# Kernel optimization log

Measured on AMD Instinct MI355X. Metric: run time of the kernel, lower is better.

The kernel has to match this reference:

```python
import jax, jax.numpy as jnp
import numpy as np

N_NODES = 50000
N_EDGES = 800000
NODE_DIM = 27
HIDDEN = 64
HEADS = 4
CTX = 32
N_BUCKETS = 7
NEG_SLOPE = 0.2


def gat_layer(x, src, dst, W, att_src, att_dst, bias, n_nodes):
    """PyG GATConv with heads=HEADS, concat=False (mean over heads), self-loops already in src/dst."""
    h = (x @ W).reshape(n_nodes, HEADS, HIDDEN)          # [N,H,F]
    a_src = jnp.einsum('nhf,hf->nh', h, att_src)          # [N,H]
    a_dst = jnp.einsum('nhf,hf->nh', h, att_dst)          # [N,H]
    e = a_src[src] + a_dst[dst]                           # [E,H]
    e = jnp.where(e >= 0, e, NEG_SLOPE * e)               # leaky_relu
    # segment softmax over incoming edges of each dst node
    m = jax.ops.segment_max(e, dst, num_segments=n_nodes)
    ex = jnp.exp(e - m[dst])
    denom = jax.ops.segment_sum(ex, dst, num_segments=n_nodes)
    alpha = ex / denom[dst]                               # [E,H]
    msg = h[src] * alpha[:, :, None]                      # [E,H,F]
    out = jax.ops.segment_sum(msg, dst, num_segments=n_nodes)  # [N,H,F]
    return out.mean(axis=1) + bias                        # [N,F]


def _glorot(key, shape, fan_in, fan_out):
    s = jnp.sqrt(6.0 / (fan_in + fan_out)).astype(jnp.float32)
    return jax.random.uniform(key, shape, jnp.float32, -s, s)


def setup_inputs() -> dict:
    key = jax.random.key(0)
    ks = jax.random.split(key, 20)
    x = jax.random.normal(ks[0], (N_NODES, NODE_DIM), jnp.float32)
    edge_index = jax.random.randint(ks[1], (2, N_EDGES), 0, N_NODES)
    donor_emb = jax.random.normal(ks[2], (1, CTX), jnp.float32)
    candidate_indices = jax.random.randint(ks[3], (8192,), 0, N_NODES)
    HF = HEADS * HIDDEN
    return {
        'x': x, 'edge_index': edge_index, 'donor_emb': donor_emb,
        'candidate_indices': candidate_indices,
        'W1': _glorot(ks[4], (NODE_DIM, HF), NODE_DIM, HF),
        'as1': _glorot(ks[5], (HEADS, HIDDEN), HIDDEN, HIDDEN),
        'ad1': _glorot(ks[6], (HEADS, HIDDEN), HIDDEN, HIDDEN),
        'b1': jnp.zeros((HIDDEN,), jnp.float32),
        'W2': _glorot(ks[7], (HIDDEN, HF), HIDDEN, HF),
        'as2': _glorot(ks[8], (HEADS, HIDDEN), HIDDEN, HIDDEN),
        'ad2': _glorot(ks[9], (HEADS, HIDDEN), HIDDEN, HIDDEN),
        'b2': jnp.zeros((HIDDEN,), jnp.float32),
        'sW1': _glorot(ks[10], (HIDDEN + CTX, HIDDEN), HIDDEN + CTX, HIDDEN),
        'sb1': jnp.zeros((HIDDEN,), jnp.float32),
        'sW2': _glorot(ks[11], (HIDDEN, 1), HIDDEN, 1),
        'sb2': jnp.zeros((1,), jnp.float32),
        'lW1': _glorot(ks[12], (HIDDEN + CTX, HIDDEN), HIDDEN + CTX, HIDDEN),
        'lb1': jnp.zeros((HIDDEN,), jnp.float32),
        'lW2': _glorot(ks[13], (HIDDEN, N_BUCKETS), HIDDEN, N_BUCKETS),
        'lb2': jnp.zeros((N_BUCKETS,), jnp.float32),
    }


def reference(x, edge_index, donor_emb, candidate_indices,
              W1, as1, ad1, b1, W2, as2, ad2, b2,
              sW1, sb1, sW2, sb2, lW1, lb1, lW2, lb2):
    n = x.shape[0]
    loops = jnp.arange(n, dtype=edge_index.dtype)
    src = jnp.concatenate([edge_index[0], loops])
    dst = jnp.concatenate([edge_index[1], loops])
    h = jax.nn.elu(gat_layer(x, src, dst, W1, as1, ad1, b1, n))
    h = jax.nn.elu(gat_layer(h, src, dst, W2, as2, ad2, b2, n))
    ctx = jnp.concatenate([h, jnp.broadcast_to(donor_emb, (n, donor_emb.shape[-1]))], axis=-1)
    ctx = ctx[candidate_indices]                         # [Ncand, hidden+ctx]
    start_logits = (jax.nn.relu(ctx @ sW1 + sb1) @ sW2 + sb2).squeeze(-1)
    pooled = ctx.mean(axis=0)
    length_logits = jax.nn.relu(pooled @ lW1 + lb1) @ lW2 + lb2
    return (start_logits, length_logits)
```

## Files before the change

kernel.cpp:

```cpp
#include <hip/hip_runtime.h>

#define N_NODES 50000
#define N_EDGES 800000
#define N_TOT   850000
#define FIN 27
#define NCAND 8192
#define CTXD 32
#define NBUCK 7
#define NEG 0.2f
#define MAXDEG 64
#define NSLICE 8
#define SL_N 6250
#define EPB 1024
#define NCHUNK 831
#define FILLB (NCHUNK * NSLICE)

typedef unsigned short ushortT;

__device__ __forceinline__ float bfu(ushortT u) { return __uint_as_float(((unsigned)u) << 16); }
__device__ __forceinline__ unsigned f2b(float f) {
    unsigned bits = __float_as_uint(f);
    return (bits + 0x7FFFu + ((bits >> 16) & 1u)) >> 16;
}
__device__ __forceinline__ int degslot(int d) { return (d & 7) * SL_N + (d >> 3); }

__global__ __launch_bounds__(256) void kernelA(
    const int* __restrict__ e_src, const int* __restrict__ e_dst,
    int* __restrict__ degS, ushortT* __restrict__ csr16,
    const float* __restrict__ x, const float* __restrict__ W1,
    const float* __restrict__ as1, const float* __restrict__ ad1,
    const float* __restrict__ W2, const float* __restrict__ as2, const float* __restrict__ ad2,
    const float* __restrict__ donor, const float* __restrict__ sW1, const float* __restrict__ sb1,
    const float* __restrict__ lW1, const float* __restrict__ lb1,
    unsigned* __restrict__ xbu, float* __restrict__ asb, float* __restrict__ adb,
    float* __restrict__ u2s, float* __restrict__ u2d,
    float* __restrict__ cs, float* __restrict__ cl, float* __restrict__ pooledP) {
    __shared__ float u1[256];
    int bid = blockIdx.x;
    int t = threadIdx.x;

    if (bid < FILLB) {
        int chunk = bid >> 3;
        int slice = bid & 7;
        int e0 = chunk * EPB;
#pragma unroll
        for (int i = 0; i < EPB / 256; i++) {
            int e = e0 + i * 256 + t;
            if (e < N_TOT) {
                int d = (e < N_EDGES) ? __builtin_nontemporal_load(e_dst + e) : (e - N_EDGES);
                if ((d & 7) == slice) {
                    int s = (e < N_EDGES) ? __builtin_nontemporal_load(e_src + e) : d;
                    int p = atomicAdd(&degS[degslot(d)], 1);
                    if (p < MAXDEG) csr16[((long)d << 6) + p] = (ushortT)s;
                }
            }
        }
    } else if (bid < FILLB + 196) {
        if (t < 4 * FIN) {
            int h = t / FIN, k = t % FIN;
            float s = 0.f;
            for (int f = 0; f < 64; f++) s += W1[k * 256 + h * 64 + f] * as1[h * 64 + f];
            u1[h * 32 + k] = s;
        } else if (t >= 128 && t < 128 + 4 * FIN) {
            int tt = t - 128;
            int h = tt / FIN, k = tt % FIN;
            float d = 0.f;
            for (int f = 0; f < 64; f++) d += W1[k * 256 + h * 64 + f] * ad1[h * 64 + f];
            u1[128 + h * 32 + k] = d;
        }
        __syncthreads();
        int n = (bid - FILLB) * 256 + t;
        if (n < N_NODES) {
            float xr[FIN];
#pragma unroll
            for (int k = 0; k < FIN; k++) xr[k] = x[(long)n * FIN + k];
            float s0 = 0, s1 = 0, s2 = 0, s3 = 0, d0 = 0, d1 = 0, d2 = 0, d3 = 0;
#pragma unroll
            for (int k = 0; k < FIN; k++) {
                float xv = xr[k];
                s0 = fmaf(xv, u1[0 * 32 + k], s0);
                s1 = fmaf(xv, u1[1 * 32 + k], s1);
                s2 = fmaf(xv, u1[2 * 32 + k], s2);
                s3 = fmaf(xv, u1[3 * 32 + k], s3);
                d0 = fmaf(xv, u1[128 + 0 * 32 + k], d0);
                d1 = fmaf(xv, u1[128 + 1 * 32 + k], d1);
                d2 = fmaf(xv, u1[128 + 2 * 32 + k], d2);
                d3 = fmaf(xv, u1[128 + 3 * 32 + k], d3);
            }
            float4 sv; sv.x = s0; sv.y = s1; sv.z = s2; sv.w = s3;
            float4 dv; dv.x = d0; dv.y = d1; dv.z = d2; dv.w = d3;
            *(float4*)(asb + n * 4) = sv;
            *(float4*)(adb + n * 4) = dv;
#pragma unroll
            for (int i = 0; i < 16; i++) {
                float a = (2 * i < FIN) ? xr[2 * i] : 0.f;
                float b = (2 * i + 1 < FIN) ? xr[2 * i + 1] : 0.f;
                xbu[(long)n * 16 + i] = f2b(a) | (f2b(b) << 16);
            }
        }
    } else {
        pooledP[t] = 0.f;
        pooledP[256 + t] = 0.f;
        {
            int h = t >> 6, k = t & 63;
            float s = 0.f, d = 0.f;
            for (int f = 0; f < 64; f++) {
                float w = W2[k * 256 + h * 64 + f];
                s += w * as2[h * 64 + f];
                d += w * ad2[h * 64 + f];
            }
            u2s[h * 64 + k] = s;
            u2d[h * 64 + k] = d;
        }
        if (t < 64) {
            float a = sb1[t];
            float b = lb1[t];
            for (int m = 0; m < CTXD; m++) {
                float d = donor[m];
                a += d * sW1[(64 + m) * 64 + t];
                b += d * lW1[(64 + m) * 64 + t];
            }
            cs[t] = a;
            cl[t] = b;
        }
    }
}

template <int FEATS, bool USECAND>
__global__ __launch_bounds__(256) void msg_kernel(
    const ushortT* __restrict__ feat, const float* __restrict__ asb,
    const float* __restrict__ adb, const int* __restrict__ degS,
    const ushortT* __restrict__ csr16, const int* __restrict__ cand,
    float* __restrict__ agg, int ndst) {
    __shared__ float wls[4][256];
    __shared__ int   sls[4][64];
    int wslot = threadIdx.x >> 6;
    int lane = threadIdx.x & 63;
    int wid = (blockIdx.x * 256 + threadIdx.x) >> 6;
    if (wid >= ndst) return;
    int dst = USECAND ? cand[wid] : wid;
    const float4 ad4 = *(const float4*)(adb + dst * 4);
    int cnt = min(degS[degslot(dst)], MAXDEG);
    float a0 = 0, a1 = 0, a2 = 0, a3 = 0;
    float d0 = 0, d1 = 0, d2 = 0, d3 = 0;
    const int f = lane & (FEATS - 1);
    {
        float w0 = 0, w1 = 0, w2 = 0, w3 = 0;
        int sj = dst;
        if (lane < cnt) {
            sj = (int)csr16[((long)dst << 6) + lane];
            const float4 as4 = *(const float4*)(asb + sj * 4);
            float e0 = as4.x + ad4.x; e0 = fmaxf(e0, NEG * e0); w0 = __expf(e0);
            float e1 = as4.y + ad4.y; e1 = fmaxf(e1, NEG * e1); w1 = __expf(e1);
            float e2 = as4.z + ad4.z; e2 = fmaxf(e2, NEG * e2); w2 = __expf(e2);
            float e3 = as4.w + ad4.w; e3 = fmaxf(e3, NEG * e3); w3 = __expf(e3);
            d0 = w0; d1 = w1; d2 = w2; d3 = w3;
        }
        float4 wv; wv.x = w0; wv.y = w1; wv.z = w2; wv.w = w3;
        *(float4*)&wls[wslot][lane * 4] = wv;
        sls[wslot][lane] = sj;
        asm volatile("" ::: "memory");
        if (FEATS == 32) {
            int iters = (cnt + 1) >> 1;
            int half = lane >> 5;
#pragma unroll 4
            for (int it = 0; it < iters; ++it) {
                int e = it * 2 + half;
                int s = sls[wslot][e];
                float4 w4 = *(const float4*)&wls[wslot][e * 4];
                float fv = bfu(feat[(long)s * FEATS + f]);
                a0 = fmaf(w4.x, fv, a0);
                a1 = fmaf(w4.y, fv, a1);
                a2 = fmaf(w4.z, fv, a2);
                a3 = fmaf(w4.w, fv, a3);
            }
        } else {
#pragma unroll 4
            for (int e = 0; e < cnt; ++e) {
                int s = sls[wslot][e];
                float4 w4 = *(const float4*)&wls[wslot][e * 4];
                float fv = bfu(feat[(long)s * FEATS + f]);
                a0 = fmaf(w4.x, fv, a0);
                a1 = fmaf(w4.y, fv, a1);
                a2 = fmaf(w4.z, fv, a2);
                a3 = fmaf(w4.w, fv, a3);
            }
        }
    }
#pragma unroll
    for (int o = 32; o > 0; o >>= 1) {
        d0 += __shfl_xor(d0, o, 64);
        d1 += __shfl_xor(d1, o, 64);
        d2 += __shfl_xor(d2, o, 64);
        d3 += __shfl_xor(d3, o, 64);
    }
    if (FEATS == 32) {
        a0 += __shfl_xor(a0, 32, 64);
        a1 += __shfl_xor(a1, 32, 64);
        a2 += __shfl_xor(a2, 32, 64);
        a3 += __shfl_xor(a3, 32, 64);
    }
    if (lane < FEATS) {
        float4 r;
        r.x = a0 * (0.25f / d0);
        r.y = a1 * (0.25f / d1);
        r.z = a2 * (0.25f / d2);
        r.w = a3 * (0.25f / d3);
        *(float4*)(agg + (long)wid * (FEATS * 4) + lane * 4) = r;
    }
}

__global__ __launch_bounds__(256) void gemm1_kernel(
    const float* __restrict__ agg1, const float* __restrict__ W1,
    const float* __restrict__ b1, ushortT* __restrict__ hmid_b) {
    __shared__ float sagg[16 * 128];
    int t = threadIdx.x;
    int n0 = blockIdx.x * 16;
    {
        const float4* src = (const float4*)(agg1 + (long)n0 * 128);
        float4* dst = (float4*)sagg;
        dst[t] = src[t];
        dst[t + 256] = src[t + 256];
    }
    __syncthreads();
    int r0 = (t >> 6) * 4;
    int f = t & 63;
    float bb = b1[f];
    float accA = bb, accB = bb, accC = bb, accD = bb;
    const float* pA = sagg + (r0 + 0) * 128;
    const float* pB = sagg + (r0 + 1) * 128;
    const float* pC = sagg + (r0 + 2) * 128;
    const float* pD = sagg + (r0 + 3) * 128;
#pragma unroll
    for (int k = 0; k < FIN; k++) {
        const float* wr = W1 + k * 256 + f;
        float w0 = wr[0], w1 = wr[64], w2 = wr[128], w3 = wr[192];
        float4 aA = *(const float4*)(pA + k * 4);
        float4 aB = *(const float4*)(pB + k * 4);
        float4 aC = *(const float4*)(pC + k * 4);
        float4 aD = *(const float4*)(pD + k * 4);
        accA = fmaf(aA.x, w0, accA); accA = fmaf(aA.y, w1, accA);
        accA = fmaf(aA.z, w2, accA); accA = fmaf(aA.w, w3, accA);
        accB = fmaf(aB.x, w0, accB); accB = fmaf(aB.y, w1, accB);
        accB = fmaf(aB.z, w2, accB); accB = fmaf(aB.w, w3, accB);
        accC = fmaf(aC.x, w0, accC); accC = fmaf(aC.y, w1, accC);
        accC = fmaf(aC.z, w2, accC); accC = fmaf(aC.w, w3, accC);
        accD = fmaf(aD.x, w0, accD); accD = fmaf(aD.y, w1, accD);
        accD = fmaf(aD.z, w2, accD); accD = fmaf(aD.w, w3, accD);
    }
    int n = n0 + r0;
    float v;
    v = accA; v = (v > 0.f) ? v : (__expf(v) - 1.f); hmid_b[(long)(n + 0) * 64 + f] = (ushortT)f2b(v);
    v = accB; v = (v > 0.f) ? v : (__expf(v) - 1.f); hmid_b[(long)(n + 1) * 64 + f] = (ushortT)f2b(v);
    v = accC; v = (v > 0.f) ? v : (__expf(v) - 1.f); hmid_b[(long)(n + 2) * 64 + f] = (ushortT)f2b(v);
    v = accD; v = (v > 0.f) ? v : (__expf(v) - 1.f); hmid_b[(long)(n + 3) * 64 + f] = (ushortT)f2b(v);
}

__global__ __launch_bounds__(256) void dots2_kernel(
    const ushortT* __restrict__ hmid_b, const float* __restrict__ u2s,
    const float* __restrict__ u2d, float* __restrict__ asb, float* __restrict__ adb) {
    int n = blockIdx.x * 256 + threadIdx.x;
    if (n >= N_NODES) return;
    float s0 = 0, s1 = 0, s2 = 0, s3 = 0, d0 = 0, d1 = 0, d2 = 0, d3 = 0;
    const uint2* hp = (const uint2*)(hmid_b + (long)n * 64);
#pragma unroll
    for (int i = 0; i < 16; i++) {
        uint2 p = hp[i];
        float vv[4];
        vv[0] = bfu((ushortT)(p.x & 0xffff));
        vv[1] = bfu((ushortT)(p.x >> 16));
        vv[2] = bfu((ushortT)(p.y & 0xffff));
        vv[3] = bfu((ushortT)(p.y >> 16));
#pragma unroll
        for (int j = 0; j < 4; j++) {
            int f = 4 * i + j;
            s0 = fmaf(vv[j], u2s[f], s0);
            s1 = fmaf(vv[j], u2s[64 + f], s1);
            s2 = fmaf(vv[j], u2s[128 + f], s2);
            s3 = fmaf(vv[j], u2s[192 + f], s3);
            d0 = fmaf(vv[j], u2d[f], d0);
            d1 = fmaf(vv[j], u2d[64 + f], d1);
            d2 = fmaf(vv[j], u2d[128 + f], d2);
            d3 = fmaf(vv[j], u2d[192 + f], d3);
        }
    }
    float4 sv; sv.x = s0; sv.y = s1; sv.z = s2; sv.w = s3;
    float4 dv; dv.x = d0; dv.y = d1; dv.z = d2; dv.w = d3;
    *(float4*)(asb + n * 4) = sv;
    *(float4*)(adb + n * 4) = dv;
}

__global__ __launch_bounds__(256) void gemm2s_kernel(
    const float* __restrict__ agg2, const float* __restrict__ W2,
    const float* __restrict__ b2, const float* __restrict__ cs,
    const float* __restrict__ sW1, const float* __restrict__ sW2,
    const float* __restrict__ sb2, float* __restrict__ out,
    float* __restrict__ pooledP) {
    __shared__ float sagg[16 * 256];
    __shared__ float hrow[4][4][64];
    __shared__ float ps[4][64];
    int t = threadIdx.x;
    int cb = blockIdx.x * 16;
    {
        const float4* src = (const float4*)(agg2 + (long)cb * 256);
        float4* dst = (float4*)sagg;
        dst[t] = src[t];
        dst[t + 256] = src[t + 256];
        dst[t + 512] = src[t + 512];
        dst[t + 768] = src[t + 768];
    }
    __syncthreads();
    int wslot = t >> 6;
    int f = t & 63;
    int r0 = wslot * 4;
    int c0 = cb + r0;
    float bb = b2[f];
    float accA = bb, accB = bb, accC = bb, accD = bb;
    const float* pA = sagg + (r0 + 0) * 256;
    const float* pB = sagg + (r0 + 1) * 256;
    const float* pC = sagg + (r0 + 2) * 256;
    const float* pD = sagg + (r0 + 3) * 256;
    for (int k = 0; k < 64; k++) {
        const float* wr = W2 + k * 256 + f;
        float w0 = wr[0], w1 = wr[64], w2 = wr[128], w3 = wr[192];
        float4 aA = *(const float4*)(pA + k * 4);
        float4 aB = *(const float4*)(pB + k * 4);
        float4 aC = *(const float4*)(pC + k * 4);
        float4 aD = *(const float4*)(pD + k * 4);
        accA = fmaf(aA.x, w0, accA); accA = fmaf(aA.y, w1, accA);
        accA = fmaf(aA.z, w2, accA); accA = fmaf(aA.w, w3, accA);
        accB = fmaf(aB.x, w0, accB); accB = fmaf(aB.y, w1, accB);
        accB = fmaf(aB.z, w2, accB); accB = fmaf(aB.w, w3, accB);
        accC = fmaf(aC.x, w0, accC); accC = fmaf(aC.y, w1, accC);
        accC = fmaf(aC.z, w2, accC); accC = fmaf(aC.w, w3, accC);
        accD = fmaf(aD.x, w0, accD); accD = fmaf(aD.y, w1, accD);
        accD = fmaf(aD.z, w2, accD); accD = fmaf(aD.w, w3, accD);
    }
    float v, vA, vB, vC, vD;
    v = accA; vA = (v > 0.f) ? v : (__expf(v) - 1.f);
    v = accB; vB = (v > 0.f) ? v : (__expf(v) - 1.f);
    v = accC; vC = (v > 0.f) ? v : (__expf(v) - 1.f);
    v = accD; vD = (v > 0.f) ? v : (__expf(v) - 1.f);
    hrow[wslot][0][f] = vA;
    hrow[wslot][1][f] = vB;
    hrow[wslot][2][f] = vC;
    hrow[wslot][3][f] = vD;
    ps[wslot][f] = vA + vB + vC + vD;
    asm volatile("" ::: "memory");
    float sw2 = sW2[f];
    float csf = cs[f];
#pragma unroll
    for (int c = 0; c < 4; c++) {
        float hid = csf;
#pragma unroll 8
        for (int k = 0; k < 64; k++) hid = fmaf(hrow[wslot][c][k], sW1[k * 64 + f], hid);
        hid = fmaxf(hid, 0.f) * sw2;
#pragma unroll
        for (int o = 32; o > 0; o >>= 1) hid += __shfl_xor(hid, o, 64);
        if (f == 0) out[c0 + c] = hid + sb2[0];
    }
    __syncthreads();
    if (t < 64)
        atomicAdd(&pooledP[(blockIdx.x & 7) * 64 + t],
                  ps[0][t] + ps[1][t] + ps[2][t] + ps[3][t]);
}


__global__ void length_kernel(const float* __restrict__ pooledP, const float* __restrict__ lW1,
                              const float* __restrict__ cl, const float* __restrict__ lW2,
                              const float* __restrict__ lb2, float* __restrict__ out) {
    __shared__ float hid[64];
    __shared__ float pl[64];
    int t = threadIdx.x;
    float pk = 0.f;
#pragma unroll
    for (int s = 0; s < 8; s++) pk += pooledP[s * 64 + t];
    pl[t] = pk * (1.f / NCAND);
    __syncthreads();
    float a = cl[t];
    for (int k = 0; k < 64; k++) a += pl[k] * lW1[k * 64 + t];
    hid[t] = fmaxf(a, 0.f);
    __syncthreads();
    if (t < NBUCK) {
        float acc = lb2[t];
        for (int j = 0; j < 64; j++) acc += hid[j] * lW2[j * NBUCK + t];
        out[NCAND + t] = acc;
    }
}

extern "C" void kernel_launch(void* const* d_in, const int* in_sizes, int n_in,
                              void* d_out, int out_size, void* d_ws, size_t ws_size,
                              hipStream_t stream) {
    const float* x     = (const float*)d_in[0];
    const int*   ei    = (const int*)d_in[1];
    const float* donor = (const float*)d_in[2];
    const int*   cand  = (const int*)d_in[3];
    const float* W1    = (const float*)d_in[4];
    const float* as1   = (const float*)d_in[5];
    const float* ad1   = (const float*)d_in[6];
    const float* b1    = (const float*)d_in[7];
    const float* W2    = (const float*)d_in[8];
    const float* as2   = (const float*)d_in[9];
    const float* ad2   = (const float*)d_in[10];
    const float* b2    = (const float*)d_in[11];
    const float* sW1   = (const float*)d_in[12];
    const float* sb1   = (const float*)d_in[13];
    const float* sW2   = (const float*)d_in[14];
    const float* sb2   = (const float*)d_in[15];
    const float* lW1   = (const float*)d_in[16];
    const float* lb1   = (const float*)d_in[17];
    const float* lW2   = (const float*)d_in[18];
    const float* lb2   = (const float*)d_in[19];
    float* out = (float*)d_out;

    float* wsf     = (float*)d_ws;
    float* agg1    = wsf;
    float* agg2    = agg1 + 6400000;
    float* asb     = agg2 + 2097152;
    float* adb     = asb + 200000;
    float* u2s     = adb + 200000;
    float* u2d     = u2s + 256;
    float* cs      = u2d + 256;
    float* cl      = cs + 64;
    float* pooledP = cl + 64;
    unsigned* xbu   = (unsigned*)(pooledP + 512);
    ushortT* hmid_b = (ushortT*)(xbu + 800000);
    int* degS = (int*)(hmid_b + 3200000);
    ushortT* csr16 = (ushortT*)(degS + 50000);

    const int* e_src = ei;
    const int* e_dst = ei + N_EDGES;

    hipMemsetAsync(degS, 0, N_NODES * sizeof(int), stream);
    kernelA<<<FILLB + 196 + 1, 256, 0, stream>>>(
        e_src, e_dst, degS, csr16, x, W1, as1, ad1, W2, as2, ad2,
        donor, sW1, sb1, lW1, lb1, xbu, asb, adb, u2s, u2d, cs, cl, pooledP);

    msg_kernel<32, false><<<(N_NODES + 3) / 4, 256, 0, stream>>>(
        (const ushortT*)xbu, asb, adb, degS, csr16, cand, agg1, N_NODES);
    gemm1_kernel<<<(N_NODES / 16), 256, 0, stream>>>(agg1, W1, b1, hmid_b);
    dots2_kernel<<<196, 256, 0, stream>>>(hmid_b, u2s, u2d, asb, adb);
    msg_kernel<64, true><<<(NCAND + 3) / 4, 256, 0, stream>>>(
        hmid_b, asb, adb, degS, csr16, cand, agg2, NCAND);
    gemm2s_kernel<<<(NCAND / 16), 256, 0, stream>>>(agg2, W2, b2, cs, sW1, sW2, sb2,
                                                    out, pooledP);
    length_kernel<<<1, 64, 0, stream>>>(pooledP, lW1, cl, lW2, lb2, out);
}
```

Baseline: 150.3 us.

## Build CSR via two-pass bucketed binning instead of global atomic scatter

Replaces the per-slice global-atomic CSR fill with a two-pass scheme. First, edges are binned by dst>>8 into 196 global buckets, with each block staging entries in shared memory and flushing them with batched atomics. A new csr_kernel then builds each 256-node CSR tile in shared memory and writes it out with coalesced stores plus a dense degree array. This cuts scattered global atomics and the 8x re-reading of edge data, but adds an extra kernel launch and an intermediate buffer that overflows (silently truncated) if a bucket exceeds its 6000-entry capacity.

```diff
diff --git a/kernel.cpp b/kernel.cpp
--- a/kernel.cpp
+++ b/kernel.cpp
@@ -9,11 +9,10 @@
 #define NBUCK 7
 #define NEG 0.2f
 #define MAXDEG 64
-#define NSLICE 8
-#define SL_N 6250
-#define EPB 1024
-#define NCHUNK 831
-#define FILLB (NCHUNK * NSLICE)
+#define NBKT 196
+#define LCAP 32
+#define BCAP 6000
+#define BINB 416
 
 typedef unsigned short ushortT;
 
@@ -22,11 +21,10 @@
     unsigned bits = __float_as_uint(f);
     return (bits + 0x7FFFu + ((bits >> 16) & 1u)) >> 16;
 }
-__device__ __forceinline__ int degslot(int d) { return (d & 7) * SL_N + (d >> 3); }
 
 __global__ __launch_bounds__(256) void kernelA(
     const int* __restrict__ e_src, const int* __restrict__ e_dst,
-    int* __restrict__ degS, ushortT* __restrict__ csr16,
+    unsigned* __restrict__ gbuf, int* __restrict__ bcnt,
     const float* __restrict__ x, const float* __restrict__ W1,
     const float* __restrict__ as1, const float* __restrict__ ad1,
     const float* __restrict__ W2, const float* __restrict__ as2, const float* __restrict__ ad2,
@@ -35,27 +33,51 @@
     unsigned* __restrict__ xbu, float* __restrict__ asb, float* __restrict__ adb,
     float* __restrict__ u2s, float* __restrict__ u2d,
     float* __restrict__ cs, float* __restrict__ cl, float* __restrict__ pooledP) {
-    __shared__ float u1[256];
+    __shared__ unsigned shbuf[NBKT * LCAP];
+    __shared__ int lcnt[NBKT];
+    __shared__ int gbase[NBKT];
     int bid = blockIdx.x;
     int t = threadIdx.x;
 
-    if (bid < FILLB) {
-        int chunk = bid >> 3;
-        int slice = bid & 7;
-        int e0 = chunk * EPB;
-#pragma unroll
-        for (int i = 0; i < EPB / 256; i++) {
+    if (bid < BINB) {
+        for (int i = t; i < NBKT; i += 256) lcnt[i] = 0;
+        __syncthreads();
+        int e0 = bid * 2048;
+#pragma unroll
+        for (int i = 0; i < 8; i++) {
             int e = e0 + i * 256 + t;
             if (e < N_TOT) {
-                int d = (e < N_EDGES) ? __builtin_nontemporal_load(e_dst + e) : (e - N_EDGES);
-                if ((d & 7) == slice) {
-                    int s = (e < N_EDGES) ? __builtin_nontemporal_load(e_src + e) : d;
-                    int p = atomicAdd(&degS[degslot(d)], 1);
-                    if (p < MAXDEG) csr16[((long)d << 6) + p] = (ushortT)s;
+                int d, s;
+                if (e < N_EDGES) { d = e_dst[e]; s = e_src[e]; }
+                else             { d = e - N_EDGES; s = d; }
+                int b = d >> 8;
+                unsigned pk = ((unsigned)(d & 255) << 16) | (unsigned)s;
+                int p = atomicAdd(&lcnt[b], 1);
+                if (p < LCAP) {
+                    shbuf[b * LCAP + p] = pk;
+                } else {
+                    int g = atomicAdd(&bcnt[b], 1);
+                    if (g < BCAP) gbuf[(long)b * BCAP + g] = pk;
                 }
             }
         }
-    } else if (bid < FILLB + 196) {
+        __syncthreads();
+        if (t < NBKT) {
+            int c = min(lcnt[t], LCAP);
+            lcnt[t] = c;
+            gbase[t] = (c > 0) ? atomicAdd(&bcnt[t], c) : 0;
+        }
+        __syncthreads();
+        int wslot = t >> 6, lane = t & 63;
+        for (int b = wslot; b < NBKT; b += 4) {
+            int c = lcnt[b];
+            if (lane < c) {
+                int pos = gbase[b] + lane;
+                if (pos < BCAP) gbuf[(long)b * BCAP + pos] = shbuf[b * LCAP + lane];
+            }
+        }
+    } else if (bid < BINB + 196) {
+        float* u1 = (float*)shbuf;
         if (t < 4 * FIN) {
             int h = t / FIN, k = t % FIN;
             float s = 0.f;
@@ -69,7 +91,7 @@
             u1[128 + h * 32 + k] = d;
         }
         __syncthreads();
-        int n = (bid - FILLB) * 256 + t;
+        int n = (bid - BINB) * 256 + t;
         if (n < N_NODES) {
             float xr[FIN];
 #pragma unroll
@@ -126,10 +148,35 @@
     }
 }
 
+__global__ __launch_bounds__(256) void csr_kernel(
+    const unsigned* __restrict__ gbuf, const int* __restrict__ bcnt,
+    ushortT* __restrict__ csr16, int* __restrict__ deg) {
+    __shared__ ushortT rows[256 * MAXDEG];
+    __shared__ int cnt[256];
+    int b = blockIdx.x;
+    int t = threadIdx.x;
+    cnt[t] = 0;
+    __syncthreads();
+    int n = min(bcnt[b], BCAP);
+    for (int i = t; i < n; i += 256) {
+        unsigned e = gbuf[(long)b * BCAP + i];
+        int dl = e >> 16;
+        int p = atomicAdd(&cnt[dl], 1);
+        if (p < MAXDEG) rows[dl * MAXDEG + p] = (ushortT)(e & 0xffff);
+    }
+    __syncthreads();
+    const unsigned* rows32 = (const unsigned*)rows;
+    unsigned* csr32 = (unsigned*)(csr16 + (long)b * 256 * MAXDEG);
+#pragma unroll
+    for (int i = 0; i < 256 * MAXDEG / 2 / 256; i++) csr32[i * 256 + t] = rows32[i * 256 + t];
+    int node = b * 256 + t;
+    if (node < N_NODES) deg[node] = min(cnt[t], MAXDEG);
+}
+
 template <int FEATS, bool USECAND>
 __global__ __launch_bounds__(256) void msg_kernel(
     const ushortT* __restrict__ feat, const float* __restrict__ asb,
-    const float* __restrict__ adb, const int* __restrict__ degS,
+    const float* __restrict__ adb, const int* __restrict__ deg,
     const ushortT* __restrict__ csr16, const int* __restrict__ cand,
     float* __restrict__ agg, int ndst) {
     __shared__ float wls[4][256];
@@ -140,7 +187,7 @@
     if (wid >= ndst) return;
     int dst = USECAND ? cand[wid] : wid;
     const float4 ad4 = *(const float4*)(adb + dst * 4);
-    int cnt = min(degS[degslot(dst)], MAXDEG);
+    int cnt = min(deg[dst], MAXDEG);
     float a0 = 0, a1 = 0, a2 = 0, a3 = 0;
     float d0 = 0, d1 = 0, d2 = 0, d3 = 0;
     const int f = lane & (FEATS - 1);
@@ -425,23 +472,26 @@
     float* pooledP = cl + 64;
     unsigned* xbu   = (unsigned*)(pooledP + 512);
     ushortT* hmid_b = (ushortT*)(xbu + 800000);
-    int* degS = (int*)(hmid_b + 3200000);
-    ushortT* csr16 = (ushortT*)(degS + 50000);
+    unsigned* gbuf  = (unsigned*)(hmid_b + 3200000);
+    int* bcnt = (int*)(gbuf + (long)NBKT * BCAP);
+    int* deg  = bcnt + 256;
+    ushortT* csr16 = (ushortT*)(deg + 50000);
 
     const int* e_src = ei;
     const int* e_dst = ei + N_EDGES;
 
-    hipMemsetAsync(degS, 0, N_NODES * sizeof(int), stream);
-    kernelA<<<FILLB + 196 + 1, 256, 0, stream>>>(
-        e_src, e_dst, degS, csr16, x, W1, as1, ad1, W2, as2, ad2,
+    hipMemsetAsync(bcnt, 0, NBKT * sizeof(int), stream);
+    kernelA<<<BINB + 196 + 1, 256, 0, stream>>>(
+        e_src, e_dst, gbuf, bcnt, x, W1, as1, ad1, W2, as2, ad2,
         donor, sW1, sb1, lW1, lb1, xbu, asb, adb, u2s, u2d, cs, cl, pooledP);
+    csr_kernel<<<NBKT, 256, 0, stream>>>(gbuf, bcnt, csr16, deg);
 
     msg_kernel<32, false><<<(N_NODES + 3) / 4, 256, 0, stream>>>(
-        (const ushortT*)xbu, asb, adb, degS, csr16, cand, agg1, N_NODES);
+        (const ushortT*)xbu, asb, adb, deg, csr16, cand, agg1, N_NODES);
     gemm1_kernel<<<(N_NODES / 16), 256, 0, stream>>>(agg1, W1, b1, hmid_b);
     dots2_kernel<<<196, 256, 0, stream>>>(hmid_b, u2s, u2d, asb, adb);
     msg_kernel<64, true><<<(NCAND + 3) / 4, 256, 0, stream>>>(
-        hmid_b, asb, adb, degS, csr16, cand, agg2, NCAND);
+        hmid_b, asb, adb, deg, csr16, cand, agg2, NCAND);
     gemm2s_kernel<<<(NCAND / 16), 256, 0, stream>>>(agg2, W2, b2, cs, sW1, sW2, sb2,
                                                     out, pooledP);
     length_kernel<<<1, 64, 0, stream>>>(pooledP, lW1, cl, lW2, lb2, out);
```

Measured after the change: 192.6 us. 1.28x slower.
